# Optimization experiments

Hardware: AMD Instinct MI355X
Metric: run time of the kernel (lower is better)

Reference implementation:

```python
import jax, jax.numpy as jnp
import numpy as np

B, N, D, H_IMG, W_IMG = 1, 6, 128, 28, 60
HB, WB = 50, 50
HEADS, DH = 4, 32
INNER = HEADS * DH  # 128 == D
Q = HB * WB
NK = N * H_IMG * W_IMG


def _ln(x, w, b, eps=1e-5):
    m = jnp.mean(x, axis=-1, keepdims=True)
    v = jnp.var(x, axis=-1, keepdims=True)
    return (x - m) * jax.lax.rsqrt(v + eps) * w + b


def setup_inputs() -> dict:
    key = jax.random.key(0)
    ks = jax.random.split(key, 20)
    s = 0.02
    inp = {
        "q": jax.random.normal(ks[0], (B, D, HB, WB), jnp.float32),
        "k": jax.random.normal(ks[1], (B, N, D, H_IMG, W_IMG), jnp.float32),
        "v": jax.random.normal(ks[2], (B, N, D, H_IMG, W_IMG), jnp.float32),
        "W_logits": jax.random.uniform(ks[3], (B, Q, NK), jnp.float32),
        "vis_flat": jax.random.randint(ks[4], (B, Q, NK), 0, 2).astype(jnp.int32),
        "skip": jax.random.normal(ks[5], (B, D, HB, WB), jnp.float32),
        # LayerNorm params
        "qn_w": jnp.ones((D,), jnp.float32), "qn_b": jnp.zeros((D,), jnp.float32),
        "kn_w": jnp.ones((D,), jnp.float32), "kn_b": jnp.zeros((D,), jnp.float32),
        "vn_w": jnp.ones((D,), jnp.float32), "vn_b": jnp.zeros((D,), jnp.float32),
        "pre_w": jnp.ones((D,), jnp.float32), "pre_b": jnp.zeros((D,), jnp.float32),
        "post_w": jnp.ones((D,), jnp.float32), "post_b": jnp.zeros((D,), jnp.float32),
        # Linear params, stored [in, out]
        "wq": jax.random.normal(ks[6], (D, INNER), jnp.float32) * s,
        "bq": jnp.zeros((INNER,), jnp.float32),
        "wk": jax.random.normal(ks[7], (D, INNER), jnp.float32) * s,
        "bk": jnp.zeros((INNER,), jnp.float32),
        "wv": jax.random.normal(ks[8], (D, INNER), jnp.float32) * s,
        "bv": jnp.zeros((INNER,), jnp.float32),
        "wp": jax.random.normal(ks[9], (INNER, D), jnp.float32) * s,
        "bp": jnp.zeros((D,), jnp.float32),
        "w1": jax.random.normal(ks[10], (D, 2 * D), jnp.float32) * s,
        "b1": jnp.zeros((2 * D,), jnp.float32),
        "w2": jax.random.normal(ks[11], (2 * D, D), jnp.float32) * s,
        "b2": jnp.zeros((D,), jnp.float32),
    }
    return inp


def reference(q, k, v, W_logits, vis_flat, skip,
              qn_w, qn_b, kn_w, kn_b, vn_w, vn_b, pre_w, pre_b, post_w, post_b,
              wq, bq, wk, bk, wv, bv, wp, bp, w1, b1, w2, b2):
    b, d, Hb, Wb = q.shape
    _, n, _, hi, wi = k.shape
    Qn = Hb * Wb
    # b d H W -> b (H W) d ; b n d h w -> b (n h w) d
    qf = q.reshape(b, d, Qn).transpose(0, 2, 1)
    kf = k.transpose(0, 1, 3, 4, 2).reshape(b, n * hi * wi, d)
    vf = v.transpose(0, 1, 3, 4, 2).reshape(b, n * hi * wi, d)
    qf = _ln(qf, qn_w, qn_b)
    kf = _ln(kf, kn_w, kn_b)
    vf = _ln(vf, vn_w, vn_b)
    qh = (qf @ wq + bq).reshape(b, Qn, HEADS, DH).transpose(0, 2, 1, 3)
    kh = (kf @ wk + bk).reshape(b, -1, HEADS, DH).transpose(0, 2, 1, 3)
    vh = (vf @ wv + bv).reshape(b, -1, HEADS, DH).transpose(0, 2, 1, 3)
    scale = DH ** (-0.5)
    logits = jnp.einsum('bhqd,bhkd->bhqk', qh, kh) * scale  # [b,h,Q,NK]
    neg_inf = jnp.finfo(logits.dtype).min
    logits = jnp.where(vis_flat[:, None] == 0, neg_inf, logits)
    logits = logits * W_logits[:, None]  # multiplicative EAF weighting
    attn = jax.nn.softmax(logits, axis=-1)
    out = jnp.einsum('bhqk,bhkd->bhqd', attn, vh)
    out = out.transpose(0, 2, 1, 3).reshape(b, Qn, INNER)
    out = out @ wp + bp
    z = out + skip.reshape(b, d, Qn).transpose(0, 2, 1)
    z = _ln(z, pre_w, pre_b)
    z = z + (jax.nn.gelu(z @ w1 + b1, approximate=False) @ w2 + b2)
    z = _ln(z, post_w, post_b)
    return z.transpose(0, 2, 1).reshape(b, d, Hb, Wb)
```

## Files before the change

kernel.cpp:

```cpp
#include <hip/hip_runtime.h>
#include <hip/hip_bf16.h>
#include <math.h>

typedef short short8 __attribute__((ext_vector_type(8)));
typedef float floatx4 __attribute__((ext_vector_type(4)));
typedef int   intx4  __attribute__((ext_vector_type(4)));

#define D 128
#define Q 2500
#define QPAD 2560
#define NK 10080
#define NKPAD 10112
#define SPLITS 35
#define CPS 9
#define OPS 163904
#define LPS 10304
#define QSCALE 0.25501268426834347f
#define NEGBIG -3.0e38f

__device__ __forceinline__ unsigned short f2bf(float f) {
    unsigned u = __float_as_uint(f);
    unsigned r = (u + 0x7fffu + ((u >> 16) & 1u)) >> 16;
    return (unsigned short)r;
}
__device__ __forceinline__ unsigned pack2bf(float lo, float hi) {
    unsigned u0 = __float_as_uint(lo) + 0x8000u;
    unsigned u1 = __float_as_uint(hi) + 0x8000u;
    return (u0 >> 16) | (u1 & 0xffff0000u);
}
__device__ __forceinline__ float bflo(unsigned u) { return __uint_as_float(u << 16); }
__device__ __forceinline__ float bfhi(unsigned u) { return __uint_as_float(u & 0xffff0000u); }

__global__ __launch_bounds__(256) void prep_kernel(
    const float* __restrict__ qi, const float* __restrict__ ki, const float* __restrict__ vi,
    const float* __restrict__ qw, const float* __restrict__ qb_,
    const float* __restrict__ kw, const float* __restrict__ kb,
    const float* __restrict__ vw, const float* __restrict__ vb,
    unsigned short* __restrict__ xq, unsigned short* __restrict__ xk,
    unsigned short* __restrict__ xv,
    const float* __restrict__ wq, const float* __restrict__ wk,
    const float* __restrict__ wv, const float* __restrict__ wp,
    const float* __restrict__ w1, const float* __restrict__ w2,
    unsigned short* __restrict__ wqT, unsigned short* __restrict__ wkT,
    unsigned short* __restrict__ wvT, unsigned short* __restrict__ wpT,
    unsigned short* __restrict__ w1T, unsigned short* __restrict__ w2T) {
    int bid = blockIdx.x, t = threadIdx.x;
    if (bid >= 715) {
        int idx = (bid - 715) * 256 + t;
        if (idx < 49152) {
            int m = idx >> 14;
            int local = idx & 16383;
            int n = local >> 7, kk = local & 127;
            const float* w = (m == 0) ? wq : ((m == 1) ? wk : wv);
            unsigned short* o = (m == 0) ? wqT : ((m == 1) ? wkT : wvT);
            o[local] = f2bf(w[kk * 128 + n]);
        } else if (idx < 65536) {
            int local = idx - 49152;
            int n = local >> 7, kk = local & 127;
            wpT[local] = f2bf(wp[kk * 128 + n]);
        } else if (idx < 98304) {
            int local = idx - 65536;
            int n = local >> 7, kk = local & 127;
            w1T[local] = f2bf(w1[kk * 256 + n]);
        } else {
            int local = idx - 98304;
            int n = local >> 8, kk = local & 255;
            w2T[local] = f2bf(w2[kk * 128 + n]);
        }
        return;
    }
    __shared__ float lds2[32 * 132];
    const float* src; unsigned short* dst; const float *g, *b;
    int S, valid;
    if (bid < 79) {
        int p0 = bid * 32;
        src = qi + p0; S = Q; dst = xq + p0 * D; g = qw; b = qb_;
        valid = Q - p0; if (valid > 32) valid = 32;
    } else if (bid < 397) {
        int tt = bid - 79;
        int n = tt / 53, tile = tt - n * 53, r = tile * 32;
        src = ki + (size_t)(n * 128) * 1680 + r; S = 1680;
        dst = xk + (n * 1680 + r) * D; g = kw; b = kb;
        valid = 1680 - r; if (valid > 32) valid = 32;
    } else {
        int tt = bid - 397;
        int n = tt / 53, tile = tt - n * 53, r = tile * 32;
        src = vi + (size_t)(n * 128) * 1680 + r; S = 1680;
        dst = xv + (n * 1680 + r) * D; g = vw; b = vb;
        valid = 1680 - r; if (valid > 32) valid = 32;
    }
    #pragma unroll
    for (int pass = 0; pass < 4; pass++) {
        int s = pass * 256 + t;
        int d = s >> 3, ps = s & 7;
        floatx4 val = {0.f, 0.f, 0.f, 0.f};
        if (ps * 4 < valid) val = *(const floatx4*)(src + (size_t)d * S + ps * 4);
        #pragma unroll
        for (int j = 0; j < 4; j++) lds2[(ps * 4 + j) * 132 + d] = val[j];
    }
    __syncthreads();
    int lane = t & 63, wvx = t >> 6;
    int pos = wvx * 8 + (lane >> 3), l7 = lane & 7;
    floatx4 x4[4];
    #pragma unroll
    for (int k = 0; k < 4; k++) x4[k] = *(const floatx4*)(&lds2[pos * 132 + l7 * 16 + k * 4]);
    float s = 0.f, ss = 0.f;
    #pragma unroll
    for (int k = 0; k < 4; k++)
        #pragma unroll
        for (int j = 0; j < 4; j++) { s += x4[k][j]; ss += x4[k][j] * x4[k][j]; }
    #pragma unroll
    for (int m = 1; m <= 4; m <<= 1) { s += __shfl_xor(s, m, 64); ss += __shfl_xor(ss, m, 64); }
    float mean = s * (1.0f / 128.0f);
    float var = ss * (1.0f / 128.0f) - mean * mean;
    float rstd = rsqrtf(var + 1e-5f);
    short8 o1, o2;
    #pragma unroll
    for (int k = 0; k < 4; k++) {
        floatx4 g4 = *(const floatx4*)(g + l7 * 16 + k * 4);
        floatx4 b4 = *(const floatx4*)(b + l7 * 16 + k * 4);
        #pragma unroll
        for (int j = 0; j < 4; j++) {
            float o = (x4[k][j] - mean) * rstd * g4[j] + b4[j];
            if (k < 2) o1[k * 4 + j] = (short)f2bf(o);
            else o2[(k - 2) * 4 + j] = (short)f2bf(o);
        }
    }
    if (pos < valid) {
        *(short8*)(dst + pos * D + l7 * 16) = o1;
        *(short8*)(dst + pos * D + l7 * 16 + 8) = o2;
    }
}

__global__ __launch_bounds__(256) void proj_kernel(
    const unsigned short* __restrict__ xq, const unsigned short* __restrict__ xk,
    const unsigned short* __restrict__ xv,
    const unsigned short* __restrict__ wqT, const unsigned short* __restrict__ wkT,
    const unsigned short* __restrict__ wvT,
    const float* __restrict__ bq, const float* __restrict__ bk, const float* __restrict__ bv,
    unsigned short* __restrict__ qh, unsigned short* __restrict__ kh,
    unsigned short* __restrict__ vhT) {
    __shared__ short vlds[128 * 72];
    int bid = blockIdx.x;
    const unsigned short *src, *wT; const float* bias; int mb, mode; float scale;
    if (bid < 40)       { mode = 0; src = xq; wT = wqT; bias = bq; mb = bid * 64; scale = QSCALE; }
    else if (bid < 198) { mode = 1; src = xk; wT = wkT; bias = bk; mb = (bid - 40) * 64; scale = 1.0f; }
    else                { mode = 2; src = xv; wT = wvT; bias = bv; mb = (bid - 198) * 64; scale = 1.0f; }
    int t = threadIdx.x, wave = t >> 6, lane = t & 63;
    int l15 = lane & 15, quad = lane >> 4;
    int m0 = mb + wave * 16;
    floatx4 acc[8];
    #pragma unroll
    for (int i = 0; i < 8; i++) acc[i] = (floatx4){0.f, 0.f, 0.f, 0.f};
    #pragma unroll
    for (int kf = 0; kf < 4; kf++) {
        short8 A = *(const short8*)(src + (m0 + l15) * D + kf * 32 + quad * 8);
        #pragma unroll
        for (int nt = 0; nt < 8; nt++) {
            short8 Bv = *(const short8*)(wT + (nt * 16 + l15) * D + kf * 32 + quad * 8);
            acc[nt] = __builtin_amdgcn_mfma_f32_16x16x32_bf16(A, Bv, acc[nt], 0, 0, 0);
        }
    }
    if (mode != 2) {
        unsigned short* dst = (mode == 0) ? qh : kh;
        #pragma unroll
        for (int nt = 0; nt < 8; nt++) {
            float bb = bias[nt * 16 + l15];
            #pragma unroll
            for (int r = 0; r < 4; r++)
                dst[(m0 + quad * 4 + r) * D + nt * 16 + l15] = f2bf((acc[nt][r] + bb) * scale);
        }
    } else {
        #pragma unroll
        for (int nt = 0; nt < 8; nt++) {
            float bb = bias[nt * 16 + l15];
            #pragma unroll
            for (int r = 0; r < 4; r++)
                vlds[(nt * 16 + l15) * 72 + (wave * 16 + quad * 4 + r)] =
                    (short)f2bf(acc[nt][r] + bb);
        }
        __syncthreads();
        int pr = t & 31, dd = t >> 5;
        int sub = pr >> 4, i = pr & 15;
        #pragma unroll
        for (int pass = 0; pass < 16; pass++) {
            int d = pass * 8 + dd;
            unsigned lo = (unsigned short)vlds[d * 72 + sub * 32 + i];
            unsigned hi = (unsigned short)vlds[d * 72 + sub * 32 + 16 + i];
            *(unsigned*)(vhT + (size_t)d * NKPAD + mb + sub * 32 + 2 * i) = lo | (hi << 16);
        }
    }
}

__global__ __launch_bounds__(256, 3) void attn_kernel(
    const unsigned short* __restrict__ qh, const unsigned short* __restrict__ kh,
    const unsigned short* __restrict__ vhT,
    const float* __restrict__ Wl, const int* __restrict__ vis,
    unsigned* __restrict__ OpartU, float* __restrict__ lpart) {
    __shared__ short Kl[2][32 * 136];
    __shared__ short Vl[2][128 * 48];
    __shared__ unsigned Pl[4][16 * 18];
    int bid = blockIdx.x;
    int split = bid % SPLITS, qt = bid / SPLITS;
    int t = threadIdx.x, wave = t >> 6, lane = t & 63;
    int l15 = lane & 15, quad = lane >> 4;
    int qb = qt * 64 + wave * 16;
    int k00 = split * (CPS * 32);

    short8 qB[4];
    #pragma unroll
    for (int h = 0; h < 4; h++)
        qB[h] = *(const short8*)(qh + (size_t)(qb + l15) * D + h * 32 + quad * 8);

    int kr = t >> 3, ks = (t & 7) * 2;
    int vd = t >> 1, vs = (t & 1) * 2;
    const uint4* ksrc = (const uint4*)(kh + (size_t)(k00 + kr) * D + ks * 8);
    const uint4* vsrc = (const uint4*)(vhT + (size_t)vd * NKPAD + k00 + vs * 8);
    short* kdst = &Kl[0][kr * 136 + ks * 8];
    short* vdst = &Vl[0][vd * 48 + vs * 8];

    int wrow = qb + l15; if (wrow >= Q) wrow = Q - 1;
    const float* wp = Wl + (size_t)wrow * NK + k00 + quad * 4;
    const int*   vp = vis + (size_t)wrow * NK + k00 + quad * 4;

    const floatx4 zf = {0.f, 0.f, 0.f, 0.f};
    floatx4 O[4][2];
    float lacc[4];
    #pragma unroll
    for (int h = 0; h < 4; h++) { O[h][0] = zf; O[h][1] = zf; lacc[h] = 0.f; }

    uint4 ka = ksrc[0], kb2 = ksrc[1];
    uint4 va = vsrc[0], vb2 = vsrc[1];
    floatx4 wc0 = *(const floatx4*)wp;
    floatx4 wc1 = *(const floatx4*)(wp + 16);
    intx4 vc0 = *(const intx4*)vp;
    intx4 vc1 = *(const intx4*)(vp + 16);
    *(uint4*)kdst = ka;       *(uint4*)(kdst + 8) = kb2;
    *(uint4*)vdst = va;       *(uint4*)(vdst + 8) = vb2;

    unsigned* pw = Pl[wave];
    #pragma unroll 1
    for (int c = 0; c < CPS; c++) {
        __syncthreads();
        int buf = c & 1;
        uint4 nka, nkb, nva, nvb;
        floatx4 wn0, wn1; intx4 vn0, vn1;
        if (c + 1 < CPS) {
            const uint4* ks2 = ksrc + (size_t)(c + 1) * 512;
            const uint4* vs2 = vsrc + (size_t)(c + 1) * 4;
            nka = ks2[0]; nkb = ks2[1];
            nva = vs2[0]; nvb = vs2[1];
            wn0 = *(const floatx4*)(wp + (c + 1) * 32);
            wn1 = *(const floatx4*)(wp + (c + 1) * 32 + 16);
            vn0 = *(const intx4*)(vp + (c + 1) * 32);
            vn1 = *(const intx4*)(vp + (c + 1) * 32 + 16);
        }
        float a2[8], b2[8];
        #pragma unroll
        for (int r = 0; r < 4; r++) {
            a2[r]     = vc0[r] ? wc0[r] : 0.f;
            b2[r]     = vc0[r] ? 0.f : wc0[r] * NEGBIG;
            a2[4 + r] = vc1[r] ? wc1[r] : 0.f;
            b2[4 + r] = vc1[r] ? 0.f : wc1[r] * NEGBIG;
        }
        const short* Kb = Kl[buf];
        const short* Vb = Vl[buf];
        #pragma unroll
        for (int h = 0; h < 4; h++) {
            short8 kA0 = *(const short8*)(Kb + l15 * 136 + h * 32 + quad * 8);
            short8 kA1 = *(const short8*)(Kb + (16 + l15) * 136 + h * 32 + quad * 8);
            floatx4 S0 = __builtin_amdgcn_mfma_f32_16x16x32_bf16(kA0, qB[h], zf, 0, 0, 0);
            floatx4 S1 = __builtin_amdgcn_mfma_f32_16x16x32_bf16(kA1, qB[h], zf, 0, 0, 0);
            float p0[4], p1[4];
            #pragma unroll
            for (int r = 0; r < 4; r++) {
                p0[r] = exp2f(S0[r] * a2[r] + b2[r]);
                p1[r] = exp2f(S1[r] * a2[4 + r] + b2[4 + r]);
                lacc[h] += p0[r] + p1[r];
            }
            pw[(quad * 2) * 18 + l15]     = pack2bf(p0[0], p0[1]);
            pw[(quad * 2 + 1) * 18 + l15] = pack2bf(p0[2], p0[3]);
            pw[(8 + quad * 2) * 18 + l15]     = pack2bf(p1[0], p1[1]);
            pw[(8 + quad * 2 + 1) * 18 + l15] = pack2bf(p1[2], p1[3]);
            union { unsigned u[4]; short8 s8; } pb;
            #pragma unroll
            for (int jj = 0; jj < 4; jj++)
                pb.u[jj] = pw[(quad * 4 + jj) * 18 + l15];
            short8 vA0 = *(const short8*)(Vb + (h * 32 + l15) * 48 + quad * 8);
            short8 vA1 = *(const short8*)(Vb + (h * 32 + 16 + l15) * 48 + quad * 8);
            O[h][0] = __builtin_amdgcn_mfma_f32_16x16x32_bf16(vA0, pb.s8, O[h][0], 0, 0, 0);
            O[h][1] = __builtin_amdgcn_mfma_f32_16x16x32_bf16(vA1, pb.s8, O[h][1], 0, 0, 0);
        }
        if (c + 1 < CPS) {
            short* kd = buf ? kdst : (kdst + 32 * 136);
            short* vd2 = buf ? vdst : (vdst + 128 * 48);
            *(uint4*)kd = nka;       *(uint4*)(kd + 8) = nkb;
            *(uint4*)vd2 = nva;      *(uint4*)(vd2 + 8) = nvb;
            wc0 = wn0; wc1 = wn1; vc0 = vn0; vc1 = vn1;
        }
    }

    int row = qb + l15;
    #pragma unroll
    for (int h = 0; h < 4; h++) {
        float lv = lacc[h];
        lv += __shfl_xor(lv, 16, 64);
        lv += __shfl_xor(lv, 32, 64);
        if (quad == 0) lpart[(size_t)split * LPS + row * 4 + h] = lv;
        #pragma unroll
        for (int tl = 0; tl < 2; tl++) {
            uint2 o2;
            o2.x = pack2bf(O[h][tl][0], O[h][tl][1]);
            o2.y = pack2bf(O[h][tl][2], O[h][tl][3]);
            *(uint2*)(OpartU + (size_t)split * OPS + ((size_t)row * 4 + h) * 16 + tl * 8 + quad * 2) = o2;
        }
    }
}

__global__ __launch_bounds__(256) void mlp_kernel(
    const unsigned* __restrict__ Opart, const float* __restrict__ lpart,
    const unsigned short* __restrict__ wpT,
    const float* __restrict__ bp, const float* __restrict__ skip,
    const float* __restrict__ pre_w, const float* __restrict__ pre_b,
    const unsigned short* __restrict__ w1T, const float* __restrict__ b1,
    const unsigned short* __restrict__ w2T, const float* __restrict__ b2,
    const float* __restrict__ post_w, const float* __restrict__ post_b,
    float* __restrict__ out) {
    __shared__ __align__(16) char smem[68608];
    short* A1l = (short*)smem;
    short* Z1 = (short*)(smem + 17408);
    short* H1 = (short*)(smem + 34816);
    float* Zout = (float*)(smem + 17408);
    unsigned* A1u = (unsigned*)smem;

    int qb = blockIdx.x * 64;
    int t = threadIdx.x, wave = t >> 6, lane = t & 63;
    int l15 = lane & 15, quad = lane >> 4;
    int m0 = wave * 16;

    {
        int row = t >> 2, he = t & 3;
        int grow = qb + row;
        float lsum = 0.f;
        #pragma unroll 5
        for (int sp = 0; sp < SPLITS; sp++) lsum += lpart[(size_t)sp * LPS + grow * 4 + he];
        float inv = 1.0f / fmaxf(lsum, 1e-30f);
        size_t base = ((size_t)grow * 4 + he) * 16;
        #pragma unroll
        for (int sl = 0; sl < 4; sl++) {
            float a0 = 0.f, a1 = 0.f, a2 = 0.f, a3 = 0.f, a4 = 0.f, a5 = 0.f, a6 = 0.f, a7 = 0.f;
            #pragma unroll 5
            for (int sp = 0; sp < SPLITS; sp++) {
                uint4 u = *(const uint4*)(Opart + (size_t)sp * OPS + base + sl * 4);
                a0 += bflo(u.x); a1 += bfhi(u.x);
                a2 += bflo(u.y); a3 += bfhi(u.y);
                a4 += bflo(u.z); a5 += bfhi(u.z);
                a6 += bflo(u.w); a7 += bfhi(u.w);
            }
            int o = row * 68 + he * 16 + sl * 4;
            A1u[o + 0] = pack2bf(a0 * inv, a1 * inv);
            A1u[o + 1] = pack2bf(a2 * inv, a3 * inv);
            A1u[o + 2] = pack2bf(a4 * inv, a5 * inv);
            A1u[o + 3] = pack2bf(a6 * inv, a7 * inv);
        }
    }
    __syncthreads();

    floatx4 z[8];
    #pragma unroll
    for (int i = 0; i < 8; i++) z[i] = (floatx4){0.f, 0.f, 0.f, 0.f};
    #pragma unroll
    for (int kf = 0; kf < 4; kf++) {
        short8 A = *(const short8*)(A1l + (m0 + l15) * 136 + kf * 32 + quad * 8);
        #pragma unroll
        for (int nt = 0; nt < 8; nt++) {
            short8 Bv = *(const short8*)(wpT + (nt * 16 + l15) * D + kf * 32 + quad * 8);
            z[nt] = __builtin_amdgcn_mfma_f32_16x16x32_bf16(A, Bv, z[nt], 0, 0, 0);
        }
    }
    float Zv[8][4];
    #pragma unroll
    for (int nt = 0; nt < 8; nt++) {
        int n = nt * 16 + l15;
        float bb = bp[n];
        #pragma unroll
        for (int r = 0; r < 4; r++) {
            int q = qb + m0 + quad * 4 + r;
            int qc = q < Q ? q : (Q - 1);
            Zv[nt][r] = z[nt][r] + bb + skip[n * Q + qc];
        }
    }
    float Zn[8][4];
    {
        #pragma unroll
        for (int r = 0; r < 4; r++) {
            float s1 = 0.f, s2 = 0.f;
            #pragma unroll
            for (int nt = 0; nt < 8; nt++) { s1 += Zv[nt][r]; s2 += Zv[nt][r] * Zv[nt][r]; }
            #pragma unroll
            for (int m = 1; m <= 8; m <<= 1) { s1 += __shfl_xor(s1, m, 64); s2 += __shfl_xor(s2, m, 64); }
            float mean = s1 * (1.0f / 128.0f);
            float var = s2 * (1.0f / 128.0f) - mean * mean;
            float rstd = rsqrtf(var + 1e-5f);
            #pragma unroll
            for (int nt = 0; nt < 8; nt++) Zn[nt][r] = (Zv[nt][r] - mean) * rstd;
        }
        #pragma unroll
        for (int nt = 0; nt < 8; nt++) {
            int n = nt * 16 + l15;
            float g = pre_w[n], be = pre_b[n];
            #pragma unroll
            for (int r = 0; r < 4; r++) {
                Zn[nt][r] = Zn[nt][r] * g + be;
                Z1[(m0 + quad * 4 + r) * 136 + n] = (short)f2bf(Zn[nt][r]);
            }
        }
    }
    {
        floatx4 h2[16];
        #pragma unroll
        for (int i = 0; i < 16; i++) h2[i] = (floatx4){0.f, 0.f, 0.f, 0.f};
        #pragma unroll
        for (int kf = 0; kf < 4; kf++) {
            short8 A = *(const short8*)(Z1 + (m0 + l15) * 136 + kf * 32 + quad * 8);
            #pragma unroll
            for (int nt = 0; nt < 16; nt++) {
                short8 Bv = *(const short8*)(w1T + (nt * 16 + l15) * D + kf * 32 + quad * 8);
                h2[nt] = __builtin_amdgcn_mfma_f32_16x16x32_bf16(A, Bv, h2[nt], 0, 0, 0);
            }
        }
        #pragma unroll
        for (int nt = 0; nt < 16; nt++) {
            int n = nt * 16 + l15;
            float bb = b1[n];
            #pragma unroll
            for (int r = 0; r < 4; r++) {
                float x = h2[nt][r] + bb;
                float gl = 0.5f * x * (1.0f + erff(x * 0.70710678118654752f));
                H1[(m0 + quad * 4 + r) * 264 + n] = (short)f2bf(gl);
            }
        }
    }
    floatx4 o3[8];
    #pragma unroll
    for (int i = 0; i < 8; i++) o3[i] = (floatx4){0.f, 0.f, 0.f, 0.f};
    #pragma unroll
    for (int kf = 0; kf < 8; kf++) {
        short8 A = *(const short8*)(H1 + (m0 + l15) * 264 + kf * 32 + quad * 8);
        #pragma unroll
        for (int nt = 0; nt < 8; nt++) {
            short8 Bv = *(const short8*)(w2T + (nt * 16 + l15) * 256 + kf * 32 + quad * 8);
            o3[nt] = __builtin_amdgcn_mfma_f32_16x16x32_bf16(A, Bv, o3[nt], 0, 0, 0);
        }
    }
    float Z2[8][4];
    #pragma unroll
    for (int nt = 0; nt < 8; nt++) {
        int n = nt * 16 + l15;
        float bb = b2[n];
        #pragma unroll
        for (int r = 0; r < 4; r++) Z2[nt][r] = Zn[nt][r] + o3[nt][r] + bb;
    }
    float Zo[8][4];
    {
        #pragma unroll
        for (int r = 0; r < 4; r++) {
            float s1 = 0.f, s2 = 0.f;
            #pragma unroll
            for (int nt = 0; nt < 8; nt++) { s1 += Z2[nt][r]; s2 += Z2[nt][r] * Z2[nt][r]; }
            #pragma unroll
            for (int m = 1; m <= 8; m <<= 1) { s1 += __shfl_xor(s1, m, 64); s2 += __shfl_xor(s2, m, 64); }
            float mean = s1 * (1.0f / 128.0f);
            float var = s2 * (1.0f / 128.0f) - mean * mean;
            float rstd = rsqrtf(var + 1e-5f);
            #pragma unroll
            for (int nt = 0; nt < 8; nt++) Zo[nt][r] = (Z2[nt][r] - mean) * rstd;
        }
        #pragma unroll
        for (int nt = 0; nt < 8; nt++) {
            int n = nt * 16 + l15;
            float g = post_w[n], be = post_b[n];
            #pragma unroll
            for (int r = 0; r < 4; r++) Zo[nt][r] = Zo[nt][r] * g + be;
        }
    }
    __syncthreads();
    #pragma unroll
    for (int nt = 0; nt < 8; nt++)
        #pragma unroll
        for (int r = 0; r < 4; r++)
            Zout[(nt * 16 + l15) * 65 + m0 + quad * 4 + r] = Zo[nt][r];
    __syncthreads();
    {
        int pl = t & 63;
        int q = qb + pl;
        if (q < Q) {
            #pragma unroll
            for (int it = 0; it < 32; it++) {
                int n = it * 4 + (t >> 6);
                out[n * Q + q] = Zout[n * 65 + pl];
            }
        }
    }
}

extern "C" void kernel_launch(void* const* d_in, const int* in_sizes, int n_in,
                              void* d_out, int out_size, void* d_ws, size_t ws_size,
                              hipStream_t stream) {
    (void)in_sizes; (void)n_in; (void)out_size; (void)ws_size;
    const float* q      = (const float*)d_in[0];
    const float* k      = (const float*)d_in[1];
    const float* v      = (const float*)d_in[2];
    const float* Wl     = (const float*)d_in[3];
    const int*   vis    = (const int*)  d_in[4];
    const float* skip   = (const float*)d_in[5];
    const float* qn_w   = (const float*)d_in[6];
    const float* qn_b   = (const float*)d_in[7];
    const float* kn_w   = (const float*)d_in[8];
    const float* kn_b   = (const float*)d_in[9];
    const float* vn_w   = (const float*)d_in[10];
    const float* vn_b   = (const float*)d_in[11];
    const float* pre_w  = (const float*)d_in[12];
    const float* pre_b  = (const float*)d_in[13];
    const float* post_w = (const float*)d_in[14];
    const float* post_b = (const float*)d_in[15];
    const float* wq     = (const float*)d_in[16];
    const float* bq     = (const float*)d_in[17];
    const float* wk     = (const float*)d_in[18];
    const float* bk     = (const float*)d_in[19];
    const float* wv     = (const float*)d_in[20];
    const float* bv     = (const float*)d_in[21];
    const float* wp     = (const float*)d_in[22];
    const float* bp     = (const float*)d_in[23];
    const float* w1     = (const float*)d_in[24];
    const float* b1     = (const float*)d_in[25];
    const float* w2     = (const float*)d_in[26];
    const float* b2     = (const float*)d_in[27];
    float* out = (float*)d_out;

    char* ws = (char*)d_ws;
    unsigned short* xq  = (unsigned short*)(ws + 0);
    unsigned short* xk  = (unsigned short*)(ws + 655360);
    unsigned short* xv  = (unsigned short*)(ws + 3244032);
    unsigned short* qh  = (unsigned short*)(ws + 5832704);
    unsigned short* kh  = (unsigned short*)(ws + 6488064);
    unsigned short* vhT = (unsigned short*)(ws + 9076736);
    unsigned short* wqT = (unsigned short*)(ws + 11665408);
    unsigned short* wkT = (unsigned short*)(ws + 11698176);
    unsigned short* wvT = (unsigned short*)(ws + 11730944);
    unsigned short* wpT = (unsigned short*)(ws + 11763712);
    unsigned short* w1T = (unsigned short*)(ws + 11796480);
    unsigned short* w2T = (unsigned short*)(ws + 11862016);
    unsigned* OpartU    = (unsigned*)(ws + 11927552);
    float* lpart        = (float*)(ws + 34874112);

    prep_kernel<<<dim3(1227), dim3(256), 0, stream>>>(
        q, k, v, qn_w, qn_b, kn_w, kn_b, vn_w, vn_b, xq, xk, xv,
        wq, wk, wv, wp, w1, w2, wqT, wkT, wvT, wpT, w1T, w2T);
    proj_kernel<<<dim3(356), dim3(256), 0, stream>>>(xq, xk, xv, wqT, wkT, wvT, bq, bk, bv,
                                                     qh, kh, vhT);
    attn_kernel<<<dim3(40 * SPLITS), dim3(256), 0, stream>>>(qh, kh, vhT, Wl, vis, OpartU, lpart);
    mlp_kernel<<<dim3(40), dim3(256), 0, stream>>>(OpartU, lpart, wpT, bp, skip,
                                                   pre_w, pre_b, w1T, b1, w2T, b2,
                                                   post_w, post_b, out);
}
```

Measured before the change: 366.7 us.

## Load K/V fragments straight from global in attention, split combine into own kernel

The attention kernel stops staging K and V tiles through double-buffered shared memory. Each wave now loads its MFMA operand fragments directly from global memory, which removes the per-chunk __syncthreads and frees LDS so occupancy can go from 3 to 4 blocks per CU. The cost is redundant global/L2 traffic: all four waves read the same K/V data, and the V fragment reads are strided. The split-K reduction also moves out of the 40-block MLP kernel into a separate 320-block combine kernel, giving that memory-bound reduction more parallelism at the price of one extra launch and an A1 round trip through global memory.

```diff
diff --git a/kernel.cpp b/kernel.cpp
--- a/kernel.cpp
+++ b/kernel.cpp
@@ -192,14 +192,12 @@
     }
 }
 
-__global__ __launch_bounds__(256, 3) void attn_kernel(
+__global__ __launch_bounds__(256, 4) void attn_kernel(
     const unsigned short* __restrict__ qh, const unsigned short* __restrict__ kh,
     const unsigned short* __restrict__ vhT,
     const float* __restrict__ Wl, const int* __restrict__ vis,
     unsigned* __restrict__ OpartU, float* __restrict__ lpart) {
-    __shared__ short Kl[2][32 * 136];
-    __shared__ short Vl[2][128 * 48];
-    __shared__ unsigned Pl[4][16 * 18];
+    __shared__ unsigned Pl[4][4][16 * 18];
     int bid = blockIdx.x;
     int split = bid % SPLITS, qt = bid / SPLITS;
     int t = threadIdx.x, wave = t >> 6, lane = t & 63;
@@ -212,12 +210,10 @@
     for (int h = 0; h < 4; h++)
         qB[h] = *(const short8*)(qh + (size_t)(qb + l15) * D + h * 32 + quad * 8);
 
-    int kr = t >> 3, ks = (t & 7) * 2;
-    int vd = t >> 1, vs = (t & 1) * 2;
-    const uint4* ksrc = (const uint4*)(kh + (size_t)(k00 + kr) * D + ks * 8);
-    const uint4* vsrc = (const uint4*)(vhT + (size_t)vd * NKPAD + k00 + vs * 8);
-    short* kdst = &Kl[0][kr * 136 + ks * 8];
-    short* vdst = &Vl[0][vd * 48 + vs * 8];
+    const unsigned short* kp0 = kh + (size_t)(k00 + l15) * D + quad * 8;
+    const unsigned short* kp1 = kp0 + 16 * D;
+    const unsigned short* vp0 = vhT + (size_t)l15 * NKPAD + k00 + quad * 8;
+    const unsigned short* vp1 = vp0 + (size_t)16 * NKPAD;
 
     int wrow = qb + l15; if (wrow >= Q) wrow = Q - 1;
     const float* wp = Wl + (size_t)wrow * NK + k00 + quad * 4;
@@ -229,27 +225,15 @@
     #pragma unroll
     for (int h = 0; h < 4; h++) { O[h][0] = zf; O[h][1] = zf; lacc[h] = 0.f; }
 
-    uint4 ka = ksrc[0], kb2 = ksrc[1];
-    uint4 va = vsrc[0], vb2 = vsrc[1];
     floatx4 wc0 = *(const floatx4*)wp;
     floatx4 wc1 = *(const floatx4*)(wp + 16);
     intx4 vc0 = *(const intx4*)vp;
     intx4 vc1 = *(const intx4*)(vp + 16);
-    *(uint4*)kdst = ka;       *(uint4*)(kdst + 8) = kb2;
-    *(uint4*)vdst = va;       *(uint4*)(vdst + 8) = vb2;
-
-    unsigned* pw = Pl[wave];
+
     #pragma unroll 1
     for (int c = 0; c < CPS; c++) {
-        __syncthreads();
-        int buf = c & 1;
-        uint4 nka, nkb, nva, nvb;
         floatx4 wn0, wn1; intx4 vn0, vn1;
         if (c + 1 < CPS) {
-            const uint4* ks2 = ksrc + (size_t)(c + 1) * 512;
-            const uint4* vs2 = vsrc + (size_t)(c + 1) * 4;
-            nka = ks2[0]; nkb = ks2[1];
-            nva = vs2[0]; nvb = vs2[1];
             wn0 = *(const floatx4*)(wp + (c + 1) * 32);
             wn1 = *(const floatx4*)(wp + (c + 1) * 32 + 16);
             vn0 = *(const intx4*)(vp + (c + 1) * 32);
@@ -263,12 +247,10 @@
             a2[4 + r] = vc1[r] ? wc1[r] : 0.f;
             b2[4 + r] = vc1[r] ? 0.f : wc1[r] * NEGBIG;
         }
-        const short* Kb = Kl[buf];
-        const short* Vb = Vl[buf];
         #pragma unroll
         for (int h = 0; h < 4; h++) {
-            short8 kA0 = *(const short8*)(Kb + l15 * 136 + h * 32 + quad * 8);
-            short8 kA1 = *(const short8*)(Kb + (16 + l15) * 136 + h * 32 + quad * 8);
+            short8 kA0 = *(const short8*)(kp0 + (size_t)c * 32 * D + h * 32);
+            short8 kA1 = *(const short8*)(kp1 + (size_t)c * 32 * D + h * 32);
             floatx4 S0 = __builtin_amdgcn_mfma_f32_16x16x32_bf16(kA0, qB[h], zf, 0, 0, 0);
             floatx4 S1 = __builtin_amdgcn_mfma_f32_16x16x32_bf16(kA1, qB[h], zf, 0, 0, 0);
             float p0[4], p1[4];
@@ -278,26 +260,21 @@
                 p1[r] = exp2f(S1[r] * a2[4 + r] + b2[4 + r]);
                 lacc[h] += p0[r] + p1[r];
             }
-            pw[(quad * 2) * 18 + l15]     = pack2bf(p0[0], p0[1]);
-            pw[(quad * 2 + 1) * 18 + l15] = pack2bf(p0[2], p0[3]);
-            pw[(8 + quad * 2) * 18 + l15]     = pack2bf(p1[0], p1[1]);
-            pw[(8 + quad * 2 + 1) * 18 + l15] = pack2bf(p1[2], p1[3]);
+            unsigned* pwh = &Pl[wave][h][0];
+            pwh[(quad * 2) * 18 + l15]     = pack2bf(p0[0], p0[1]);
+            pwh[(quad * 2 + 1) * 18 + l15] = pack2bf(p0[2], p0[3]);
+            pwh[(8 + quad * 2) * 18 + l15]     = pack2bf(p1[0], p1[1]);
+            pwh[(8 + quad * 2 + 1) * 18 + l15] = pack2bf(p1[2], p1[3]);
             union { unsigned u[4]; short8 s8; } pb;
             #pragma unroll
             for (int jj = 0; jj < 4; jj++)
-                pb.u[jj] = pw[(quad * 4 + jj) * 18 + l15];
-            short8 vA0 = *(const short8*)(Vb + (h * 32 + l15) * 48 + quad * 8);
-            short8 vA1 = *(const short8*)(Vb + (h * 32 + 16 + l15) * 48 + quad * 8);
+                pb.u[jj] = pwh[(quad * 4 + jj) * 18 + l15];
+            short8 vA0 = *(const short8*)(vp0 + (size_t)(h * 32) * NKPAD + c * 32);
+            short8 vA1 = *(const short8*)(vp1 + (size_t)(h * 32) * NKPAD + c * 32);
             O[h][0] = __builtin_amdgcn_mfma_f32_16x16x32_bf16(vA0, pb.s8, O[h][0], 0, 0, 0);
             O[h][1] = __builtin_amdgcn_mfma_f32_16x16x32_bf16(vA1, pb.s8, O[h][1], 0, 0, 0);
         }
-        if (c + 1 < CPS) {
-            short* kd = buf ? kdst : (kdst + 32 * 136);
-            short* vd2 = buf ? vdst : (vdst + 128 * 48);
-            *(uint4*)kd = nka;       *(uint4*)(kd + 8) = nkb;
-            *(uint4*)vd2 = nva;      *(uint4*)(vd2 + 8) = nvb;
-            wc0 = wn0; wc1 = wn1; vc0 = vn0; vc1 = vn1;
-        }
+        wc0 = wn0; wc1 = wn1; vc0 = vn0; vc1 = vn1;
     }
 
     int row = qb + l15;
@@ -317,8 +294,35 @@
     }
 }
 
+__global__ __launch_bounds__(128) void combine_kernel(
+    const unsigned* __restrict__ Opart, const float* __restrict__ lpart,
+    unsigned* __restrict__ A1u) {
+    int tid = blockIdx.x * 128 + threadIdx.x;
+    int sl = tid & 3, he = (tid >> 2) & 3, grow = tid >> 4;
+    float lsum = 0.f;
+    #pragma unroll 7
+    for (int sp = 0; sp < SPLITS; sp++) lsum += lpart[(size_t)sp * LPS + grow * 4 + he];
+    float inv = 1.0f / fmaxf(lsum, 1e-30f);
+    size_t base = ((size_t)grow * 4 + he) * 16 + sl * 4;
+    float a0 = 0.f, a1 = 0.f, a2 = 0.f, a3 = 0.f, a4 = 0.f, a5 = 0.f, a6 = 0.f, a7 = 0.f;
+    #pragma unroll 7
+    for (int sp = 0; sp < SPLITS; sp++) {
+        uint4 u = *(const uint4*)(Opart + (size_t)sp * OPS + base);
+        a0 += bflo(u.x); a1 += bfhi(u.x);
+        a2 += bflo(u.y); a3 += bfhi(u.y);
+        a4 += bflo(u.z); a5 += bfhi(u.z);
+        a6 += bflo(u.w); a7 += bfhi(u.w);
+    }
+    uint4 o;
+    o.x = pack2bf(a0 * inv, a1 * inv);
+    o.y = pack2bf(a2 * inv, a3 * inv);
+    o.z = pack2bf(a4 * inv, a5 * inv);
+    o.w = pack2bf(a6 * inv, a7 * inv);
+    *(uint4*)(A1u + (size_t)grow * 64 + he * 16 + sl * 4) = o;
+}
+
 __global__ __launch_bounds__(256) void mlp_kernel(
-    const unsigned* __restrict__ Opart, const float* __restrict__ lpart,
+    const unsigned short* __restrict__ A1,
     const unsigned short* __restrict__ wpT,
     const float* __restrict__ bp, const float* __restrict__ skip,
     const float* __restrict__ pre_w, const float* __restrict__ pre_b,
@@ -326,52 +330,22 @@
     const unsigned short* __restrict__ w2T, const float* __restrict__ b2,
     const float* __restrict__ post_w, const float* __restrict__ post_b,
     float* __restrict__ out) {
-    __shared__ __align__(16) char smem[68608];
-    short* A1l = (short*)smem;
-    short* Z1 = (short*)(smem + 17408);
-    short* H1 = (short*)(smem + 34816);
-    float* Zout = (float*)(smem + 17408);
-    unsigned* A1u = (unsigned*)smem;
+    __shared__ __align__(16) char smem[51200];
+    short* Z1 = (short*)smem;
+    short* H1 = (short*)(smem + 17408);
+    float* Zout = (float*)smem;
 
     int qb = blockIdx.x * 64;
     int t = threadIdx.x, wave = t >> 6, lane = t & 63;
     int l15 = lane & 15, quad = lane >> 4;
     int m0 = wave * 16;
 
-    {
-        int row = t >> 2, he = t & 3;
-        int grow = qb + row;
-        float lsum = 0.f;
-        #pragma unroll 5
-        for (int sp = 0; sp < SPLITS; sp++) lsum += lpart[(size_t)sp * LPS + grow * 4 + he];
-        float inv = 1.0f / fmaxf(lsum, 1e-30f);
-        size_t base = ((size_t)grow * 4 + he) * 16;
-        #pragma unroll
-        for (int sl = 0; sl < 4; sl++) {
-            float a0 = 0.f, a1 = 0.f, a2 = 0.f, a3 = 0.f, a4 = 0.f, a5 = 0.f, a6 = 0.f, a7 = 0.f;
-            #pragma unroll 5
-            for (int sp = 0; sp < SPLITS; sp++) {
-                uint4 u = *(const uint4*)(Opart + (size_t)sp * OPS + base + sl * 4);
-                a0 += bflo(u.x); a1 += bfhi(u.x);
-                a2 += bflo(u.y); a3 += bfhi(u.y);
-                a4 += bflo(u.z); a5 += bfhi(u.z);
-                a6 += bflo(u.w); a7 += bfhi(u.w);
-            }
-            int o = row * 68 + he * 16 + sl * 4;
-            A1u[o + 0] = pack2bf(a0 * inv, a1 * inv);
-            A1u[o + 1] = pack2bf(a2 * inv, a3 * inv);
-            A1u[o + 2] = pack2bf(a4 * inv, a5 * inv);
-            A1u[o + 3] = pack2bf(a6 * inv, a7 * inv);
-        }
-    }
-    __syncthreads();
-
     floatx4 z[8];
     #pragma unroll
     for (int i = 0; i < 8; i++) z[i] = (floatx4){0.f, 0.f, 0.f, 0.f};
     #pragma unroll
     for (int kf = 0; kf < 4; kf++) {
-        short8 A = *(const short8*)(A1l + (m0 + l15) * 136 + kf * 32 + quad * 8);
+        short8 A = *(const short8*)(A1 + (size_t)(qb + m0 + l15) * 128 + kf * 32 + quad * 8);
         #pragma unroll
         for (int nt = 0; nt < 8; nt++) {
             short8 Bv = *(const short8*)(wpT + (nt * 16 + l15) * D + kf * 32 + quad * 8);
@@ -553,6 +527,7 @@
     unsigned short* w2T = (unsigned short*)(ws + 11862016);
     unsigned* OpartU    = (unsigned*)(ws + 11927552);
     float* lpart        = (float*)(ws + 34874112);
+    unsigned* A1u       = (unsigned*)(ws + 0);
 
     prep_kernel<<<dim3(1227), dim3(256), 0, stream>>>(
         q, k, v, qn_w, qn_b, kn_w, kn_b, vn_w, vn_b, xq, xk, xv,
@@ -560,7 +535,8 @@
     proj_kernel<<<dim3(356), dim3(256), 0, stream>>>(xq, xk, xv, wqT, wkT, wvT, bq, bk, bv,
                                                      qh, kh, vhT);
     attn_kernel<<<dim3(40 * SPLITS), dim3(256), 0, stream>>>(qh, kh, vhT, Wl, vis, OpartU, lpart);
-    mlp_kernel<<<dim3(40), dim3(256), 0, stream>>>(OpartU, lpart, wpT, bp, skip,
+    combine_kernel<<<dim3(320), dim3(128), 0, stream>>>(OpartU, lpart, A1u);
+    mlp_kernel<<<dim3(40), dim3(256), 0, stream>>>((const unsigned short*)A1u, wpT, bp, skip,
                                                    pre_w, pre_b, w1T, b1, w2T, b2,
                                                    post_w, post_b, out);
 }
```

Measured after the change: 494.9 us. 1.35x slower.
